# Performance work log

Measured on AMD Instinct MI355X. Metric: run time of the kernel, lower is better.

## Reference

```python
import jax, jax.numpy as jnp
import numpy as np

B, C, H, W, WS, SH, NH, P = 64, 512, 28, 28, 7, 3, 16, 10
MLP_H = 2048
EPS = 1e-5
NW = (H // WS) * (W // WS)  # 16 windows per image
N = P + WS * WS             # 59 tokens per window
HEAD_D = C // NH
SCALE = HEAD_D ** -0.5


def _rel_pos_index(ws):
    coords = np.stack(np.meshgrid(np.arange(ws), np.arange(ws), indexing='ij')).reshape(2, -1)
    rel = (coords[:, :, None] - coords[:, None, :]).transpose(1, 2, 0)
    rel[..., 0] += ws - 1
    rel[..., 1] += ws - 1
    rel[..., 0] *= 2 * ws - 1
    return rel.sum(-1)  # (ws*ws, ws*ws)


def _attn_mask(h, w, ws, shift):
    img = np.zeros((h, w), dtype=np.float32)
    slices = (slice(0, -ws), slice(-ws, -shift), slice(-shift, None))
    cnt = 0
    for hs in slices:
        for wsl in slices:
            img[hs, wsl] = cnt
            cnt += 1
    mw = img.reshape(h // ws, ws, w // ws, ws).transpose(0, 2, 1, 3).reshape(-1, ws * ws)
    diff = mw[:, None, :] - mw[:, :, None]
    return np.where(diff != 0, -100.0, 0.0).astype(np.float32)  # (nW, ws*ws, ws*ws)


_RPI = jnp.asarray(_rel_pos_index(WS))
_MASK = jnp.asarray(_attn_mask(H, W, WS, SH))


def _ln(x, g, b):
    mu = jnp.mean(x, -1, keepdims=True)
    var = jnp.mean((x - mu) ** 2, -1, keepdims=True)
    return (x - mu) * jax.lax.rsqrt(var + EPS) * g + b


def _window_partition(x, ws):
    b, h, w, c = x.shape
    x = x.reshape(b, h // ws, ws, w // ws, ws, c).transpose(0, 1, 3, 2, 4, 5)
    return x.reshape(-1, ws, ws, c)


def _window_reverse(win, ws, h, w):
    b = win.shape[0] // ((h // ws) * (w // ws))
    x = win.reshape(b, h // ws, w // ws, ws, ws, -1).transpose(0, 1, 3, 2, 4, 5)
    return x.reshape(b, h, w, -1)


def setup_inputs() -> dict:
    key = jax.random.key(0)
    ks = jax.random.split(key, 8)
    d = {
        'x': jax.random.normal(ks[0], (B, P + H * W, C), jnp.float32),
        'g1': jnp.ones((C,), jnp.float32),
        'b1': jnp.zeros((C,), jnp.float32),
        'qkv_w': jax.random.normal(ks[1], (3 * C, C), jnp.float32) * 0.02,
        'qkv_b': jnp.zeros((3 * C,), jnp.float32),
        'rpb_table': jax.random.normal(ks[2], ((2 * WS - 1) ** 2, NH), jnp.float32) * 0.02,
        'proj_w': jax.random.normal(ks[3], (C, C), jnp.float32) * 0.02,
        'proj_b': jnp.zeros((C,), jnp.float32),
        'g2': jnp.ones((C,), jnp.float32),
        'b2': jnp.zeros((C,), jnp.float32),
        'fc1_w': jax.random.normal(ks[4], (MLP_H, C), jnp.float32) * 0.02,
        'fc1_b': jnp.zeros((MLP_H,), jnp.float32),
        'fc2_w': jax.random.normal(ks[5], (C, MLP_H), jnp.float32) * 0.02,
        'fc2_b': jnp.zeros((C,), jnp.float32),
    }
    return d


def _block(x, g1, b1, qkv_w, qkv_b, rpb_table, proj_w, proj_b, g2, b2, fc1_w, fc1_b, fc2_w, fc2_b):
    prompt = x[:, :P, :]                       # (B, P, C)
    x = x[:, P:, :]                            # (B, H*W, C)
    shortcut = x
    xn = _ln(x, g1, b1).reshape(B, H, W, C)
    # cyclic shift
    xn = jnp.roll(xn, shift=(-SH, -SH), axis=(1, 2))
    xw = _window_partition(xn, WS).reshape(-1, WS * WS, C)  # (B*nW, 49, C)
    # prompt padding (matches torch expand(nW,...).reshape order: index = w*B + b)
    pw = jnp.broadcast_to(prompt[None], (NW, B, P, C)).reshape(-1, P, C)
    xw = jnp.concatenate([pw, xw], axis=1)     # (B*nW, N, C)
    B_ = B * NW
    # attention
    qkv = (xw @ qkv_w.T + qkv_b).reshape(B_, N, 3, NH, HEAD_D).transpose(2, 0, 3, 1, 4)
    q, k, v = qkv[0], qkv[1], qkv[2]
    attn = jnp.einsum('bhnd,bhmd->bhnm', q * SCALE, k)  # (B_, NH, N, N)
    bias = rpb_table[_RPI.reshape(-1)].reshape(WS * WS, WS * WS, NH).transpose(2, 0, 1)
    bias = jnp.pad(bias, ((0, 0), (P, 0), (P, 0)))       # (NH, N, N)
    mask = jnp.pad(_MASK, ((0, 0), (P, 0), (P, 0)))      # (nW, N, N)
    attn = attn + bias[None]
    attn = attn.reshape(B, NW, NH, N, N) + mask[None, :, None]
    attn = jax.nn.softmax(attn.reshape(B_, NH, N, N), axis=-1)
    out = jnp.einsum('bhnm,bhmd->bhnd', attn, v).transpose(0, 2, 1, 3).reshape(B_, N, C)
    out = out @ proj_w.T + proj_b
    # drop prompts, un-window, un-shift
    out = out[:, P:, :].reshape(-1, WS, WS, C)
    xs = _window_reverse(out, WS, H, W)
    xs = jnp.roll(xs, shift=(SH, SH), axis=(1, 2)).reshape(B, H * W, C)
    x = shortcut + xs
    # MLP (exact GELU, as torch nn.GELU)
    h = _ln(x, g2, b2)
    h = jax.nn.gelu(h @ fc1_w.T + fc1_b, approximate=False)
    h = h @ fc2_w.T + fc2_b
    return x + h


def reference(x, g1, b1, qkv_w, qkv_b, rpb_table, proj_w, proj_b, g2, b2, fc1_w, fc1_b, fc2_w, fc2_b):
    return _block(x, g1, b1, qkv_w, qkv_b, rpb_table, proj_w, proj_b, g2, b2, fc1_w, fc1_b, fc2_w, fc2_b)
```

## Files before the change

### kernel.cpp

```cpp
#include <hip/hip_runtime.h>
#include <stdint.h>

typedef unsigned short u16;
typedef unsigned int u32;
typedef __attribute__((ext_vector_type(8))) short short8;
typedef __attribute__((ext_vector_type(4))) float f32x4;

__device__ __forceinline__ u16 f2bf(float f) {
  u32 u = __builtin_bit_cast(u32, f);
  u32 r = u + 0x7FFFu + ((u >> 16) & 1u);
  return (u16)(r >> 16);
}

__device__ __forceinline__ void gl_lds16(const void* g, void* l) {
  __builtin_amdgcn_global_load_lds((__attribute__((address_space(1))) void*)g,
                                   (__attribute__((address_space(3))) void*)l,
                                   16, 0, 0);
}

__device__ __forceinline__ float gelu_fast(float v) {
  float u = 0.7978845608028654f * (v + 0.044715f * v * v * v);
  float a = fabsf(u);
  float e = __expf(-2.0f * a);
  float t = (1.0f - e) / (1.0f + e);
  float th = copysignf(t, u);
  return 0.5f * v * (1.0f + th);
}

__global__ __launch_bounds__(256) void cvt_bf16(const float* __restrict__ in,
                                                u16* __restrict__ out, int n4) {
  int idx = blockIdx.x * 256 + threadIdx.x;
  if (idx < n4) {
    float4 v = ((const float4*)in)[idx];
    u32 lo = (u32)f2bf(v.x) | ((u32)f2bf(v.y) << 16);
    u32 hi = (u32)f2bf(v.z) | ((u32)f2bf(v.w) << 16);
    ((uint2*)out)[idx] = make_uint2(lo, hi);
  }
}

__global__ __launch_bounds__(256) void ln1_kernel(const float* __restrict__ x,
                                                  const float* __restrict__ g,
                                                  const float* __restrict__ bta,
                                                  u16* __restrict__ xcat) {
  int wave = threadIdx.x >> 6, lane = threadIdx.x & 63;
  int row = blockIdx.x * 4 + wave;
  const float* src;
  bool do_ln;
  if (row < 640) {
    int bb = row / 10, p = row - bb * 10;
    src = x + ((size_t)bb * 794 + p) * 512;
    do_ln = false;
  } else {
    int r2 = row - 640;
    int i = r2 / 49, t = r2 - i * 49;
    int bb = i >> 4, nw = i & 15;
    int tr = t / 7, tc = t - tr * 7;
    int hh = (nw >> 2) * 7 + tr + 3; if (hh >= 28) hh -= 28;
    int ww = (nw & 3) * 7 + tc + 3;  if (ww >= 28) ww -= 28;
    src = x + ((size_t)bb * 794 + 10 + hh * 28 + ww) * 512;
    do_ln = true;
  }
  float4 v0 = ((const float4*)src)[lane * 2];
  float4 v1 = ((const float4*)src)[lane * 2 + 1];
  float vals[8] = {v0.x, v0.y, v0.z, v0.w, v1.x, v1.y, v1.z, v1.w};
  u16 ob[8];
  if (do_ln) {
    float s = 0.f, s2 = 0.f;
#pragma unroll
    for (int j = 0; j < 8; ++j) { s += vals[j]; s2 += vals[j] * vals[j]; }
#pragma unroll
    for (int o = 32; o > 0; o >>= 1) { s += __shfl_xor(s, o); s2 += __shfl_xor(s2, o); }
    float mu = s * (1.0f / 512.0f);
    float var = s2 * (1.0f / 512.0f) - mu * mu;
    float inv = rsqrtf(var + 1e-5f);
    float4 ga = ((const float4*)g)[lane * 2], gb = ((const float4*)g)[lane * 2 + 1];
    float4 ba = ((const float4*)bta)[lane * 2], bb2 = ((const float4*)bta)[lane * 2 + 1];
    float gv[8] = {ga.x, ga.y, ga.z, ga.w, gb.x, gb.y, gb.z, gb.w};
    float bv[8] = {ba.x, ba.y, ba.z, ba.w, bb2.x, bb2.y, bb2.z, bb2.w};
#pragma unroll
    for (int j = 0; j < 8; ++j) ob[j] = f2bf((vals[j] - mu) * inv * gv[j] + bv[j]);
  } else {
#pragma unroll
    for (int j = 0; j < 8; ++j) ob[j] = f2bf(vals[j]);
  }
  u32 w0 = (u32)ob[0] | ((u32)ob[1] << 16);
  u32 w1 = (u32)ob[2] | ((u32)ob[3] << 16);
  u32 w2 = (u32)ob[4] | ((u32)ob[5] << 16);
  u32 w3 = (u32)ob[6] | ((u32)ob[7] << 16);
  ((uint4*)(xcat + (size_t)row * 512))[lane] = make_uint4(w0, w1, w2, w3);
}

__global__ __launch_bounds__(256) void ln2_kernel(const float* __restrict__ xn,
                                                  const float* __restrict__ g,
                                                  const float* __restrict__ bta,
                                                  u16* __restrict__ outb) {
  int wave = threadIdx.x >> 6, lane = threadIdx.x & 63;
  size_t row = (size_t)blockIdx.x * 4 + wave;
  const float* src = xn + row * 512;
  float4 v0 = ((const float4*)src)[lane * 2];
  float4 v1 = ((const float4*)src)[lane * 2 + 1];
  float vals[8] = {v0.x, v0.y, v0.z, v0.w, v1.x, v1.y, v1.z, v1.w};
  float s = 0.f, s2 = 0.f;
#pragma unroll
  for (int j = 0; j < 8; ++j) { s += vals[j]; s2 += vals[j] * vals[j]; }
#pragma unroll
  for (int o = 32; o > 0; o >>= 1) { s += __shfl_xor(s, o); s2 += __shfl_xor(s2, o); }
  float mu = s * (1.0f / 512.0f);
  float var = s2 * (1.0f / 512.0f) - mu * mu;
  float inv = rsqrtf(var + 1e-5f);
  float4 ga = ((const float4*)g)[lane * 2], gb = ((const float4*)g)[lane * 2 + 1];
  float4 ba = ((const float4*)bta)[lane * 2], bb2 = ((const float4*)bta)[lane * 2 + 1];
  float gv[8] = {ga.x, ga.y, ga.z, ga.w, gb.x, gb.y, gb.z, gb.w};
  float bv[8] = {ba.x, ba.y, ba.z, ba.w, bb2.x, bb2.y, bb2.z, bb2.w};
  u16 ob[8];
#pragma unroll
  for (int j = 0; j < 8; ++j) ob[j] = f2bf((vals[j] - mu) * inv * gv[j] + bv[j]);
  u32 w0 = (u32)ob[0] | ((u32)ob[1] << 16);
  u32 w1 = (u32)ob[2] | ((u32)ob[3] << 16);
  u32 w2 = (u32)ob[4] | ((u32)ob[5] << 16);
  u32 w3 = (u32)ob[6] | ((u32)ob[7] << 16);
  ((uint4*)(outb + row * 512))[lane] = make_uint4(w0, w1, w2, w3);
}

template <int EPI>
__global__ __launch_bounds__(512, 2) void gemm256(const u16* __restrict__ A,
                                                  const u16* __restrict__ Wt,
                                                  const float* __restrict__ bias,
                                                  u16* __restrict__ outb,
                                                  float* __restrict__ outf,
                                                  const float* __restrict__ res,
                                                  int M, int N, int K, int Ntiles) {
  __shared__ __align__(16) u16 Asm[4][256 * 32];
  __shared__ __align__(16) u16 Bsm[4][256 * 32];
  const int tid = threadIdx.x;
  const int lane = tid & 63;
  const int wv = tid >> 6;
  const int wm = wv >> 2, wn = wv & 3;
  const int lr = lane & 15;
  const int qh = lane >> 4;
  const int swz8 = (qh ^ ((lr >> 1) & 3)) << 3;

  const int nwg = gridDim.x;
  const int qx = nwg >> 3, rx = nwg & 7;
  const int xcd = blockIdx.x & 7, local = blockIdx.x >> 3;
  const int swz = (xcd < rx ? xcd * (qx + 1) : rx * (qx + 1) + (xcd - rx) * qx) + local;
  const int mt = swz / Ntiles, nt = swz - mt * Ntiles;
  const int tm = mt * 256, tn = nt * 256;

  f32x4 acc[8][4];
#pragma unroll
  for (int m = 0; m < 8; ++m)
#pragma unroll
    for (int n = 0; n < 4; ++n)
#pragma unroll
      for (int e = 0; e < 4; ++e) acc[m][n][e] = 0.f;

  const int sr = tid >> 2;
  const int sl = tid & 3;
  const int scol = (sl ^ ((sr >> 1) & 3)) << 3;
  const u16* Ap0 = A + (size_t)(tm + sr) * K + scol;
  const u16* Ap1 = A + (size_t)(tm + 128 + sr) * K + scol;
  const u16* Bp0 = Wt + (size_t)(tn + sr) * K + scol;
  const u16* Bp1 = Wt + (size_t)(tn + 128 + sr) * K + scol;

#define STAGE_A(buf, k0)                          \
  do {                                            \
    u16* d = &Asm[buf][tid * 8];                  \
    gl_lds16(Ap0 + (k0), d);                      \
    gl_lds16(Ap1 + (k0), d + 4096);               \
  } while (0)
#define STAGE_B(buf, k0)                          \
  do {                                            \
    u16* d = &Bsm[buf][tid * 8];                  \
    gl_lds16(Bp0 + (k0), d);                      \
    gl_lds16(Bp1 + (k0), d + 4096);               \
  } while (0)

  const int NT = K >> 5;

  STAGE_A(0, 0);  STAGE_B(0, 0);
  STAGE_A(1, 32); STAGE_B(1, 32);
  STAGE_A(2, 64); STAGE_B(2, 64);
  asm volatile("s_waitcnt vmcnt(8)" ::: "memory");
  __builtin_amdgcn_s_barrier();

  for (int t = 0; t < NT; ++t) {
    const int b = t & 3;
    const u16* Ab = &Asm[b][0];
    const u16* Bb = &Bsm[b][0];
    const int pf = t + 3;
    const int pb = pf & 3;
    const int pk = pf << 5;

    short8 bv[4], avlo[4];
#pragma unroll
    for (int n = 0; n < 4; ++n)
      bv[n] = *(const short8*)&Bb[(wn * 64 + n * 16 + lr) * 32 + swz8];
#pragma unroll
    for (int m = 0; m < 4; ++m)
      avlo[m] = *(const short8*)&Ab[(wm * 128 + m * 16 + lr) * 32 + swz8];
    if (pf < NT) STAGE_A(pb, pk);
    asm volatile("" ::: "memory");
    __builtin_amdgcn_s_barrier();
    asm volatile("s_waitcnt lgkmcnt(0)" ::: "memory");
    __builtin_amdgcn_sched_barrier(0);
    __builtin_amdgcn_s_setprio(1);
#pragma unroll
    for (int m = 0; m < 4; ++m)
#pragma unroll
      for (int n = 0; n < 4; ++n)
        acc[m][n] = __builtin_amdgcn_mfma_f32_16x16x32_bf16(avlo[m], bv[n], acc[m][n], 0, 0, 0);
    __builtin_amdgcn_s_setprio(0);
    __builtin_amdgcn_s_barrier();

    short8 avhi[4];
#pragma unroll
    for (int m = 0; m < 4; ++m)
      avhi[m] = *(const short8*)&Ab[(wm * 128 + (m + 4) * 16 + lr) * 32 + swz8];
    if (pf < NT) STAGE_B(pb, pk);
    if (t <= NT - 4)      asm volatile("s_waitcnt vmcnt(8)" ::: "memory");
    else if (t == NT - 3) asm volatile("s_waitcnt vmcnt(4)" ::: "memory");
    else if (t == NT - 2) asm volatile("s_waitcnt vmcnt(0)" ::: "memory");
    asm volatile("" ::: "memory");
    __builtin_amdgcn_s_barrier();
    asm volatile("s_waitcnt lgkmcnt(0)" ::: "memory");
    __builtin_amdgcn_sched_barrier(0);
    __builtin_amdgcn_s_setprio(1);
#pragma unroll
    for (int m = 0; m < 4; ++m)
#pragma unroll
      for (int n = 0; n < 4; ++n)
        acc[m + 4][n] = __builtin_amdgcn_mfma_f32_16x16x32_bf16(avhi[m], bv[n], acc[m + 4][n], 0, 0, 0);
    __builtin_amdgcn_s_setprio(0);
    __builtin_amdgcn_s_barrier();
  }
#undef STAGE_A
#undef STAGE_B

  float bcol[4];
#pragma unroll
  for (int n = 0; n < 4; ++n) bcol[n] = bias[tn + wn * 64 + n * 16 + lr];

#pragma unroll
  for (int m = 0; m < 8; ++m) {
#pragma unroll
    for (int r2 = 0; r2 < 4; ++r2) {
      int grow = tm + wm * 128 + m * 16 + qh * 4 + r2;
      if (grow >= M) continue;
      if (EPI == 1) {
        int i = grow / 49, t = grow - i * 49;
        int bb = i >> 4, nw = i & 15;
        int tr = t / 7, tc = t - tr * 7;
        int hh = (nw >> 2) * 7 + tr + 3; if (hh >= 28) hh -= 28;
        int ww = (nw & 3) * 7 + tc + 3;  if (ww >= 28) ww -= 28;
        size_t dstr = ((size_t)bb * 784 + hh * 28 + ww) * 512;
        size_t srcr = ((size_t)bb * 794 + 10 + hh * 28 + ww) * 512;
#pragma unroll
        for (int n = 0; n < 4; ++n) {
          int gcol = tn + wn * 64 + n * 16 + lr;
          float v = acc[m][n][r2] + bcol[n];
          outf[dstr + gcol] = v + res[srcr + gcol];
        }
      } else {
#pragma unroll
        for (int n = 0; n < 4; ++n) {
          int gcol = tn + wn * 64 + n * 16 + lr;
          float v = acc[m][n][r2] + bcol[n];
          if (EPI == 0) {
            outb[(size_t)grow * N + gcol] = f2bf(v);
          } else if (EPI == 2) {
            outb[(size_t)grow * N + gcol] = f2bf(gelu_fast(v));
          } else {
            outf[(size_t)grow * N + gcol] = v + res[(size_t)grow * 512 + gcol];
          }
        }
      }
    }
  }
}

__global__ __launch_bounds__(64) void attn_kernel(const u16* __restrict__ Y,
                                                  const float* __restrict__ rpb,
                                                  u16* __restrict__ outp) {
  __shared__ __align__(16) u16 Plds[64 * 64];
  __shared__ __align__(16) u16 Vt[32 * 64];
  __shared__ float biasl[169];
  const int lane = threadIdx.x;
  const int i = blockIdx.x >> 4;
  const int hd = blockIdx.x & 15;
  const int bp = i & 63;
  const int nw = i & 15;
  const int hi = nw >> 2, wi = nw & 3;
  const int lr = lane & 15;
  const int lk = (lane >> 4) * 8;

  for (int j = lane; j < 169; j += 64) biasl[j] = rpb[j * 16 + hd];

  short8 qf[4], kf[4];
#pragma unroll
  for (int m = 0; m < 4; ++m) {
    int t = m * 16 + lr;
    size_t r = (t < 10) ? (size_t)(bp * 10 + t) : (size_t)(640 + i * 49 + (t - 10));
    const u16* base = Y + r * 1536 + hd * 32 + lk;
    if (t < 59) {
      qf[m] = *(const short8*)(base);
      kf[m] = *(const short8*)(base + 512);
    } else {
#pragma unroll
      for (int e = 0; e < 8; ++e) { qf[m][e] = 0; kf[m][e] = 0; }
    }
  }
  {
    int t = lane;
    if (t < 59) {
      size_t r = (t < 10) ? (size_t)(bp * 10 + t) : (size_t)(640 + i * 49 + (t - 10));
      const u16* vp = Y + r * 1536 + 1024 + hd * 32;
      short8 vv0 = *(const short8*)(vp);
      short8 vv1 = *(const short8*)(vp + 8);
      short8 vv2 = *(const short8*)(vp + 16);
      short8 vv3 = *(const short8*)(vp + 24);
#pragma unroll
      for (int e = 0; e < 8; ++e) {
        Vt[e * 64 + t] = (u16)vv0[e];
        Vt[(8 + e) * 64 + t] = (u16)vv1[e];
        Vt[(16 + e) * 64 + t] = (u16)vv2[e];
        Vt[(24 + e) * 64 + t] = (u16)vv3[e];
      }
    } else {
      for (int d = 0; d < 32; ++d) Vt[d * 64 + t] = 0;
    }
  }

  f32x4 s[4][4];
#pragma unroll
  for (int m = 0; m < 4; ++m)
#pragma unroll
    for (int n = 0; n < 4; ++n)
#pragma unroll
      for (int r2 = 0; r2 < 4; ++r2) s[m][n][r2] = 0.f;
#pragma unroll
  for (int m = 0; m < 4; ++m)
#pragma unroll
    for (int n = 0; n < 4; ++n)
      s[m][n] = __builtin_amdgcn_mfma_f32_16x16x32_bf16(qf[m], kf[n], s[m][n], 0, 0, 0);

  __syncthreads();

  const float SCALE = 0.17677669529663687f;
  const int rgrp = lane >> 4;
#pragma unroll
  for (int m = 0; m < 4; ++m) {
#pragma unroll
    for (int r2 = 0; r2 < 4; ++r2) {
      int rn = m * 16 + rgrp * 4 + r2;
      int qa = rn - 10;
      int qra = qa / 7, qca = qa - qra * 7;
      int regA = 0;
      if (qa >= 0 && qa < 49) {
        int ha = hi * 7 + qra, wa = wi * 7 + qca;
        regA = (ha < 21 ? 0 : (ha < 25 ? 1 : 2)) * 3 + (wa < 21 ? 0 : (wa < 25 ? 1 : 2));
      }
      float vloc[4];
      float mx = -3.0e38f;
#pragma unroll
      for (int n = 0; n < 4; ++n) {
        int cm = n * 16 + lr;
        float v;
        if (cm >= 59) {
          v = -3.0e38f;
        } else {
          v = s[m][n][r2] * SCALE;
          if (rn >= 10 && rn < 59 && cm >= 10) {
            int kb = cm - 10;
            int krb = kb / 7, kcb = kb - krb * 7;
            v += biasl[(qra - krb + 6) * 13 + (qca - kcb + 6)];
            int hb = hi * 7 + krb, wb = wi * 7 + kcb;
            int regB = (hb < 21 ? 0 : (hb < 25 ? 1 : 2)) * 3 + (wb < 21 ? 0 : (wb < 25 ? 1 : 2));
            if (regA != regB) v -= 100.0f;
          }
        }
        vloc[n] = v;
        mx = fmaxf(mx, v);
      }
#pragma unroll
      for (int o = 8; o > 0; o >>= 1) mx = fmaxf(mx, __shfl_xor(mx, o));
      float sum = 0.f;
#pragma unroll
      for (int n = 0; n < 4; ++n) {
        float e = __expf(vloc[n] - mx);
        vloc[n] = e;
        sum += e;
      }
#pragma unroll
      for (int o = 8; o > 0; o >>= 1) sum += __shfl_xor(sum, o);
      float inv = 1.0f / sum;
#pragma unroll
      for (int n = 0; n < 4; ++n)
        Plds[rn * 64 + n * 16 + lr] = f2bf(vloc[n] * inv);
    }
  }

  __syncthreads();

  f32x4 o[4][2];
#pragma unroll
  for (int m = 0; m < 4; ++m)
#pragma unroll
    for (int j = 0; j < 2; ++j)
#pragma unroll
      for (int r2 = 0; r2 < 4; ++r2) o[m][j][r2] = 0.f;
#pragma unroll
  for (int ks = 0; ks < 2; ++ks) {
    short8 pf[4], vf[2];
#pragma unroll
    for (int m = 0; m < 4; ++m)
      pf[m] = *(const short8*)&Plds[(m * 16 + lr) * 64 + ks * 32 + lk];
#pragma unroll
    for (int j = 0; j < 2; ++j)
      vf[j] = *(const short8*)&Vt[(j * 16 + lr) * 64 + ks * 32 + lk];
#pragma unroll
    for (int m = 0; m < 4; ++m)
#pragma unroll
      for (int j = 0; j < 2; ++j)
        o[m][j] = __builtin_amdgcn_mfma_f32_16x16x32_bf16(pf[m], vf[j], o[m][j], 0, 0, 0);
  }

#pragma unroll
  for (int m = 0; m < 4; ++m) {
#pragma unroll
    for (int r2 = 0; r2 < 4; ++r2) {
      int rn = m * 16 + rgrp * 4 + r2;
      if (rn >= 10 && rn < 59) {
        size_t row = (size_t)i * 49 + (rn - 10);
        u16* op = outp + row * 512 + hd * 32;
        op[lr] = f2bf(o[m][0][r2]);
        op[16 + lr] = f2bf(o[m][1][r2]);
      }
    }
  }
}

extern "C" void kernel_launch(void* const* d_in, const int* in_sizes, int n_in,
                              void* d_out, int out_size, void* d_ws, size_t ws_size,
                              hipStream_t stream) {
  const float* x = (const float*)d_in[0];
  const float* g1 = (const float*)d_in[1];
  const float* b1 = (const float*)d_in[2];
  const float* qkv_w = (const float*)d_in[3];
  const float* qkv_b = (const float*)d_in[4];
  const float* rpb = (const float*)d_in[5];
  const float* proj_w = (const float*)d_in[6];
  const float* proj_b = (const float*)d_in[7];
  const float* g2 = (const float*)d_in[8];
  const float* b2 = (const float*)d_in[9];
  const float* fc1_w = (const float*)d_in[10];
  const float* fc1_b = (const float*)d_in[11];
  const float* fc2_w = (const float*)d_in[12];
  const float* fc2_b = (const float*)d_in[13];
  float* out = (float*)d_out;

  char* ws = (char*)d_ws;
  u16* qkv_wb = (u16*)(ws + 0);
  u16* proj_wb = (u16*)(ws + 1572864);
  u16* fc1_wb = (u16*)(ws + 2097152);
  u16* fc2_wb = (u16*)(ws + 4194304);
  u16* xcat = (u16*)(ws + 6291456);
  u16* y = (u16*)(ws + 58327040);
  u16* attnv = (u16*)(ws + 214433792);
  float* xnew = (float*)(ws + 265814016);
  u16* hin = xcat;
  u16* hmid = y;

  cvt_bf16<<<768, 256, 0, stream>>>(qkv_w, qkv_wb, 196608);
  cvt_bf16<<<256, 256, 0, stream>>>(proj_w, proj_wb, 65536);
  cvt_bf16<<<1024, 256, 0, stream>>>(fc1_w, fc1_wb, 262144);
  cvt_bf16<<<1024, 256, 0, stream>>>(fc2_w, fc2_wb, 262144);

  ln1_kernel<<<12704, 256, 0, stream>>>(x, g1, b1, xcat);

  gemm256<0><<<199 * 6, 512, 0, stream>>>(xcat, qkv_wb, qkv_b, y, nullptr, nullptr,
                                          50816, 1536, 512, 6);

  attn_kernel<<<16384, 64, 0, stream>>>(y, rpb, attnv);

  gemm256<1><<<196 * 2, 512, 0, stream>>>(attnv, proj_wb, proj_b, nullptr, xnew, x,
                                          50176, 512, 512, 2);

  ln2_kernel<<<12544, 256, 0, stream>>>(xnew, g2, b2, hin);

  gemm256<2><<<196 * 8, 512, 0, stream>>>(hin, fc1_wb, fc1_b, hmid, nullptr, nullptr,
                                          50176, 2048, 512, 8);

  gemm256<3><<<196 * 2, 512, 0, stream>>>(hmid, fc2_wb, fc2_b, nullptr, out, xnew,
                                          50176, 512, 2048, 2);
}
```

Baseline: 809.0 us.

## Make GEMMs persistent with cross-tile prefetch pipeline

The GEMM kernel becomes persistent: a fixed grid of workgroups loops over output tiles in strides of the grid size. The load pipeline keeps prefetching the next tile's K-slices while the current tile's epilogue runs, so the ramp-up and drain per tile are hidden. The inner step is also simplified to a single barrier-wait phase that loads all A fragments at once, instead of the split lo/hi halves. The risks are tile imbalance across the fixed grid (for example 1194 tiles on 256 blocks, or 392 tiles on 196 blocks for proj), higher register pressure from loading 8 A fragments at once, and reliance on NT being a power of two for the mask arithmetic.

```diff
diff --git a/kernel.cpp b/kernel.cpp
--- a/kernel.cpp
+++ b/kernel.cpp
@@ -123,13 +123,14 @@
 }
 
 template <int EPI>
-__global__ __launch_bounds__(512, 2) void gemm256(const u16* __restrict__ A,
-                                                  const u16* __restrict__ Wt,
-                                                  const float* __restrict__ bias,
-                                                  u16* __restrict__ outb,
-                                                  float* __restrict__ outf,
-                                                  const float* __restrict__ res,
-                                                  int M, int N, int K, int Ntiles) {
+__global__ __launch_bounds__(512, 2) void gemm256p(const u16* __restrict__ A,
+                                                   const u16* __restrict__ Wt,
+                                                   const float* __restrict__ bias,
+                                                   u16* __restrict__ outb,
+                                                   float* __restrict__ outf,
+                                                   const float* __restrict__ res,
+                                                   int M, int N, int K, int Ntiles,
+                                                   int tilesTot) {
   __shared__ __align__(16) u16 Asm[4][256 * 32];
   __shared__ __align__(16) u16 Bsm[4][256 * 32];
   const int tid = threadIdx.x;
@@ -140,143 +141,146 @@
   const int qh = lane >> 4;
   const int swz8 = (qh ^ ((lr >> 1) & 3)) << 3;
 
-  const int nwg = gridDim.x;
-  const int qx = nwg >> 3, rx = nwg & 7;
+  const int G = gridDim.x;
+  const int qx = G >> 3, rx = G & 7;
   const int xcd = blockIdx.x & 7, local = blockIdx.x >> 3;
-  const int swz = (xcd < rx ? xcd * (qx + 1) : rx * (qx + 1) + (xcd - rx) * qx) + local;
-  const int mt = swz / Ntiles, nt = swz - mt * Ntiles;
-  const int tm = mt * 256, tn = nt * 256;
-
-  f32x4 acc[8][4];
-#pragma unroll
-  for (int m = 0; m < 8; ++m)
-#pragma unroll
-    for (int n = 0; n < 4; ++n)
-#pragma unroll
-      for (int e = 0; e < 4; ++e) acc[m][n][e] = 0.f;
+  const int pb = (xcd < rx ? xcd * (qx + 1) : rx * (qx + 1) + (xcd - rx) * qx) + local;
+
+  const int NT = K >> 5;
+  const int NTm1 = NT - 1;
+  const int tpb = (tilesTot - pb + G - 1) / G;
+  const int stepsTot = tpb * NT;
+
+  int curTile = pb;
+  int mt = curTile / Ntiles, nt = curTile - mt * Ntiles;
+  int tm = mt << 8, tn = nt << 8;
 
   const int sr = tid >> 2;
   const int sl = tid & 3;
   const int scol = (sl ^ ((sr >> 1) & 3)) << 3;
-  const u16* Ap0 = A + (size_t)(tm + sr) * K + scol;
-  const u16* Ap1 = A + (size_t)(tm + 128 + sr) * K + scol;
-  const u16* Bp0 = Wt + (size_t)(tn + sr) * K + scol;
-  const u16* Bp1 = Wt + (size_t)(tn + 128 + sr) * K + scol;
-
-#define STAGE_A(buf, k0)                          \
-  do {                                            \
-    u16* d = &Asm[buf][tid * 8];                  \
-    gl_lds16(Ap0 + (k0), d);                      \
-    gl_lds16(Ap1 + (k0), d + 4096);               \
+  int stageTile = pb;
+  const u16 *Ap0, *Ap1, *Bp0, *Bp1;
+  auto setStagePtrs = [&](int tIdx) {
+    int smt = tIdx / Ntiles, snt = tIdx - smt * Ntiles;
+    size_t stm = (size_t)(smt << 8), stn = (size_t)(snt << 8);
+    Ap0 = A + (stm + sr) * K + scol;
+    Ap1 = A + (stm + 128 + sr) * K + scol;
+    Bp0 = Wt + (stn + sr) * K + scol;
+    Bp1 = Wt + (stn + 128 + sr) * K + scol;
+  };
+  setStagePtrs(pb);
+
+#define STAGE(s_)                                           \
+  do {                                                      \
+    int b_ = (s_) & 3;                                      \
+    int k0_ = ((s_) & NTm1) << 5;                           \
+    gl_lds16(Ap0 + k0_, &Asm[b_][tid * 8]);                 \
+    gl_lds16(Ap1 + k0_, &Asm[b_][tid * 8 + 4096]);          \
+    gl_lds16(Bp0 + k0_, &Bsm[b_][tid * 8]);                 \
+    gl_lds16(Bp1 + k0_, &Bsm[b_][tid * 8 + 4096]);          \
   } while (0)
-#define STAGE_B(buf, k0)                          \
-  do {                                            \
-    u16* d = &Bsm[buf][tid * 8];                  \
-    gl_lds16(Bp0 + (k0), d);                      \
-    gl_lds16(Bp1 + (k0), d + 4096);               \
-  } while (0)
-
-  const int NT = K >> 5;
-
-  STAGE_A(0, 0);  STAGE_B(0, 0);
-  STAGE_A(1, 32); STAGE_B(1, 32);
-  STAGE_A(2, 64); STAGE_B(2, 64);
-  asm volatile("s_waitcnt vmcnt(8)" ::: "memory");
-  __builtin_amdgcn_s_barrier();
-
-  for (int t = 0; t < NT; ++t) {
-    const int b = t & 3;
+
+  f32x4 acc[8][4];
+#pragma unroll
+  for (int m = 0; m < 8; ++m)
+#pragma unroll
+    for (int n = 0; n < 4; ++n)
+#pragma unroll
+      for (int e = 0; e < 4; ++e) acc[m][n][e] = 0.f;
+
+  STAGE(0);
+  STAGE(1);
+  STAGE(2);
+
+  for (int s = 0; s < stepsTot; ++s) {
+    __builtin_amdgcn_s_barrier();
+    asm volatile("" ::: "memory");
+    if (s + 3 < stepsTot) {
+      if (((s + 3) & NTm1) == 0) { stageTile += G; setStagePtrs(stageTile); }
+      STAGE(s + 3);
+      asm volatile("s_waitcnt vmcnt(8)" ::: "memory");
+    } else if (s == stepsTot - 3) {
+      asm volatile("s_waitcnt vmcnt(8)" ::: "memory");
+    } else if (s == stepsTot - 2) {
+      asm volatile("s_waitcnt vmcnt(4)" ::: "memory");
+    } else {
+      asm volatile("s_waitcnt vmcnt(0)" ::: "memory");
+    }
+    __builtin_amdgcn_s_barrier();
+    asm volatile("" ::: "memory");
+
+    const int b = s & 3;
     const u16* Ab = &Asm[b][0];
     const u16* Bb = &Bsm[b][0];
-    const int pf = t + 3;
-    const int pb = pf & 3;
-    const int pk = pf << 5;
-
-    short8 bv[4], avlo[4];
+    short8 av[8], bv[4];
+#pragma unroll
+    for (int m = 0; m < 8; ++m)
+      av[m] = *(const short8*)&Ab[(wm * 128 + m * 16 + lr) * 32 + swz8];
 #pragma unroll
     for (int n = 0; n < 4; ++n)
       bv[n] = *(const short8*)&Bb[(wn * 64 + n * 16 + lr) * 32 + swz8];
-#pragma unroll
-    for (int m = 0; m < 4; ++m)
-      avlo[m] = *(const short8*)&Ab[(wm * 128 + m * 16 + lr) * 32 + swz8];
-    if (pf < NT) STAGE_A(pb, pk);
-    asm volatile("" ::: "memory");
-    __builtin_amdgcn_s_barrier();
-    asm volatile("s_waitcnt lgkmcnt(0)" ::: "memory");
-    __builtin_amdgcn_sched_barrier(0);
     __builtin_amdgcn_s_setprio(1);
 #pragma unroll
-    for (int m = 0; m < 4; ++m)
+    for (int m = 0; m < 8; ++m)
 #pragma unroll
       for (int n = 0; n < 4; ++n)
-        acc[m][n] = __builtin_amdgcn_mfma_f32_16x16x32_bf16(avlo[m], bv[n], acc[m][n], 0, 0, 0);
+        acc[m][n] = __builtin_amdgcn_mfma_f32_16x16x32_bf16(av[m], bv[n], acc[m][n], 0, 0, 0);
     __builtin_amdgcn_s_setprio(0);
-    __builtin_amdgcn_s_barrier();
-
-    short8 avhi[4];
-#pragma unroll
-    for (int m = 0; m < 4; ++m)
-      avhi[m] = *(const short8*)&Ab[(wm * 128 + (m + 4) * 16 + lr) * 32 + swz8];
-    if (pf < NT) STAGE_B(pb, pk);
-    if (t <= NT - 4)      asm volatile("s_waitcnt vmcnt(8)" ::: "memory");
-    else if (t == NT - 3) asm volatile("s_waitcnt vmcnt(4)" ::: "memory");
-    else if (t == NT - 2) asm volatile("s_waitcnt vmcnt(0)" ::: "memory");
-    asm volatile("" ::: "memory");
-    __builtin_amdgcn_s_barrier();
-    asm volatile("s_waitcnt lgkmcnt(0)" ::: "memory");
-    __builtin_amdgcn_sched_barrier(0);
-    __builtin_amdgcn_s_setprio(1);
-#pragma unroll
-    for (int m = 0; m < 4; ++m)
-#pragma unroll
-      for (int n = 0; n < 4; ++n)
-        acc[m + 4][n] = __builtin_amdgcn_mfma_f32_16x16x32_bf16(avhi[m], bv[n], acc[m + 4][n], 0, 0, 0);
-    __builtin_amdgcn_s_setprio(0);
-    __builtin_amdgcn_s_barrier();
-  }
-#undef STAGE_A
-#undef STAGE_B
-
-  float bcol[4];
-#pragma unroll
-  for (int n = 0; n < 4; ++n) bcol[n] = bias[tn + wn * 64 + n * 16 + lr];
-
-#pragma unroll
-  for (int m = 0; m < 8; ++m) {
-#pragma unroll
-    for (int r2 = 0; r2 < 4; ++r2) {
-      int grow = tm + wm * 128 + m * 16 + qh * 4 + r2;
-      if (grow >= M) continue;
-      if (EPI == 1) {
-        int i = grow / 49, t = grow - i * 49;
-        int bb = i >> 4, nw = i & 15;
-        int tr = t / 7, tc = t - tr * 7;
-        int hh = (nw >> 2) * 7 + tr + 3; if (hh >= 28) hh -= 28;
-        int ww = (nw & 3) * 7 + tc + 3;  if (ww >= 28) ww -= 28;
-        size_t dstr = ((size_t)bb * 784 + hh * 28 + ww) * 512;
-        size_t srcr = ((size_t)bb * 794 + 10 + hh * 28 + ww) * 512;
-#pragma unroll
-        for (int n = 0; n < 4; ++n) {
-          int gcol = tn + wn * 64 + n * 16 + lr;
-          float v = acc[m][n][r2] + bcol[n];
-          outf[dstr + gcol] = v + res[srcr + gcol];
-        }
-      } else {
-#pragma unroll
-        for (int n = 0; n < 4; ++n) {
-          int gcol = tn + wn * 64 + n * 16 + lr;
-          float v = acc[m][n][r2] + bcol[n];
-          if (EPI == 0) {
-            outb[(size_t)grow * N + gcol] = f2bf(v);
-          } else if (EPI == 2) {
-            outb[(size_t)grow * N + gcol] = f2bf(gelu_fast(v));
+
+    if ((s & NTm1) == NTm1) {
+      float bcol[4];
+#pragma unroll
+      for (int n = 0; n < 4; ++n) bcol[n] = bias[tn + wn * 64 + n * 16 + lr];
+#pragma unroll
+      for (int m = 0; m < 8; ++m) {
+#pragma unroll
+        for (int r2 = 0; r2 < 4; ++r2) {
+          int grow = tm + wm * 128 + m * 16 + qh * 4 + r2;
+          if (grow >= M) continue;
+          if (EPI == 1) {
+            int i = grow / 49, t = grow - i * 49;
+            int bb = i >> 4, nw = i & 15;
+            int tr = t / 7, tc = t - tr * 7;
+            int hh = (nw >> 2) * 7 + tr + 3; if (hh >= 28) hh -= 28;
+            int ww = (nw & 3) * 7 + tc + 3;  if (ww >= 28) ww -= 28;
+            size_t dstr = ((size_t)bb * 784 + hh * 28 + ww) * 512;
+            size_t srcr = ((size_t)bb * 794 + 10 + hh * 28 + ww) * 512;
+#pragma unroll
+            for (int n = 0; n < 4; ++n) {
+              int gcol = tn + wn * 64 + n * 16 + lr;
+              float v = acc[m][n][r2] + bcol[n];
+              outf[dstr + gcol] = v + res[srcr + gcol];
+            }
           } else {
-            outf[(size_t)grow * N + gcol] = v + res[(size_t)grow * 512 + gcol];
+#pragma unroll
+            for (int n = 0; n < 4; ++n) {
+              int gcol = tn + wn * 64 + n * 16 + lr;
+              float v = acc[m][n][r2] + bcol[n];
+              if (EPI == 0) {
+                outb[(size_t)grow * N + gcol] = f2bf(v);
+              } else if (EPI == 2) {
+                outb[(size_t)grow * N + gcol] = f2bf(gelu_fast(v));
+              } else {
+                outf[(size_t)grow * N + gcol] = v + res[(size_t)grow * 512 + gcol];
+              }
+            }
           }
         }
       }
+#pragma unroll
+      for (int m = 0; m < 8; ++m)
+#pragma unroll
+        for (int n = 0; n < 4; ++n)
+#pragma unroll
+          for (int e = 0; e < 4; ++e) acc[m][n][e] = 0.f;
+      curTile += G;
+      if (curTile < tilesTot) {
+        mt = curTile / Ntiles; nt = curTile - mt * Ntiles;
+        tm = mt << 8; tn = nt << 8;
+      }
     }
   }
+#undef STAGE
 }
 
 __global__ __launch_bounds__(64) void attn_kernel(const u16* __restrict__ Y,
@@ -478,19 +482,19 @@
 
   ln1_kernel<<<12704, 256, 0, stream>>>(x, g1, b1, xcat);
 
-  gemm256<0><<<199 * 6, 512, 0, stream>>>(xcat, qkv_wb, qkv_b, y, nullptr, nullptr,
-                                          50816, 1536, 512, 6);
+  gemm256p<0><<<256, 512, 0, stream>>>(xcat, qkv_wb, qkv_b, y, nullptr, nullptr,
+                                       50816, 1536, 512, 6, 1194);
 
   attn_kernel<<<16384, 64, 0, stream>>>(y, rpb, attnv);
 
-  gemm256<1><<<196 * 2, 512, 0, stream>>>(attnv, proj_wb, proj_b, nullptr, xnew, x,
-                                          50176, 512, 512, 2);
+  gemm256p<1><<<196, 512, 0, stream>>>(attnv, proj_wb, proj_b, nullptr, xnew, x,
+                                       50176, 512, 512, 2, 392);
 
   ln2_kernel<<<12544, 256, 0, stream>>>(xnew, g2, b2, hin);
 
-  gemm256<2><<<196 * 8, 512, 0, stream>>>(hin, fc1_wb, fc1_b, hmid, nullptr, nullptr,
-                                          50176, 2048, 512, 8);
-
-  gemm256<3><<<196 * 2, 512, 0, stream>>>(hmid, fc2_wb, fc2_b, nullptr, out, xnew,
-                                          50176, 512, 2048, 2);
-}
+  gemm256p<2><<<256, 512, 0, stream>>>(hin, fc1_wb, fc1_b, hmid, nullptr, nullptr,
+                                       50176, 2048, 512, 8, 1568);
+
+  gemm256p<3><<<392, 512, 0, stream>>>(hmid, fc2_wb, fc2_b, nullptr, out, xnew,
+                                       50176, 512, 2048, 2, 392);
+}
```

Result: slower. 875.3 us (+8.2%).
